# Kernel tuning notes

Measured on AMD Instinct MI355X. Metric: run time of the kernel, lower is better.

The kernel has to match this reference:

```python
import jax, jax.numpy as jnp
import numpy as np

B, DIM, H, W = 16, 512, 32, 32
C = 256          # internal channels = int(512*0.5)
HEADS = 4        # max(1, 256//64)
KD = 32          # key_dim = int(64*0.5)
HD = 64          # head_dim = 256//4
SCALE = KD ** -0.5


def _silu(x):
    return x * jax.nn.sigmoid(x)


def conv1x1(x, Wm, s, b, act):
    # 1x1 conv + folded eval-mode BN (scale/shift) + optional SiLU
    y = jnp.einsum('bchw,oc->bohw', x, Wm)
    y = y * s[None, :, None, None] + b[None, :, None, None]
    return _silu(y) if act else y


def dwconv3(x, Wd, s, b):
    # depthwise 3x3 conv (groups = channels) + BN scale/shift, no act
    y = jax.lax.conv_general_dilated(
        x, Wd, window_strides=(1, 1), padding='SAME',
        feature_group_count=x.shape[1],
        dimension_numbers=('NCHW', 'OIHW', 'NCHW'))
    return y * s[None, :, None, None] + b[None, :, None, None]


def _mk_conv(key, c_out, c_in, k=1):
    k1, k2, k3 = jax.random.split(key, 3)
    fan_in = c_in * k * k
    if k == 1:
        Wm = jax.random.normal(k1, (c_out, c_in), jnp.float32) * fan_in ** -0.5
    else:
        Wm = jax.random.normal(k1, (c_out, c_in, k, k), jnp.float32) * fan_in ** -0.5
    s = jax.random.uniform(k2, (c_out,), jnp.float32, 0.5, 1.5)
    b = 0.1 * jax.random.normal(k3, (c_out,), jnp.float32)
    return Wm, s, b


def setup_inputs() -> dict:
    key = jax.random.key(0)
    ks = jax.random.split(key, 8)
    x = jax.random.normal(ks[0], (B, DIM, H, W), jnp.float32)
    W_cv1, s_cv1, b_cv1 = _mk_conv(ks[1], 2 * C, DIM)
    W_qkv, s_qkv, b_qkv = _mk_conv(ks[2], C + 2 * HEADS * KD, C)  # 512 out
    W_proj, s_proj, b_proj = _mk_conv(ks[3], C, C)
    # depthwise 3x3: OIHW with I=1, groups=C
    W_pe, s_pe, b_pe = _mk_conv(ks[4], C, 1, k=3)
    W_ffn1, s_ffn1, b_ffn1 = _mk_conv(ks[5], 2 * C, C)
    W_ffn2, s_ffn2, b_ffn2 = _mk_conv(ks[6], C, 2 * C)
    W_cv2, s_cv2, b_cv2 = _mk_conv(ks[7], DIM, 2 * C)
    return {
        'x': x,
        'W_cv1': W_cv1, 's_cv1': s_cv1, 'b_cv1': b_cv1,
        'W_qkv': W_qkv, 's_qkv': s_qkv, 'b_qkv': b_qkv,
        'W_proj': W_proj, 's_proj': s_proj, 'b_proj': b_proj,
        'W_pe': W_pe, 's_pe': s_pe, 'b_pe': b_pe,
        'W_ffn1': W_ffn1, 's_ffn1': s_ffn1, 'b_ffn1': b_ffn1,
        'W_ffn2': W_ffn2, 's_ffn2': s_ffn2, 'b_ffn2': b_ffn2,
        'W_cv2': W_cv2, 's_cv2': s_cv2, 'b_cv2': b_cv2,
    }


def reference(x,
              W_cv1, s_cv1, b_cv1,
              W_qkv, s_qkv, b_qkv,
              W_proj, s_proj, b_proj,
              W_pe, s_pe, b_pe,
              W_ffn1, s_ffn1, b_ffn1,
              W_ffn2, s_ffn2, b_ffn2,
              W_cv2, s_cv2, b_cv2):
    bsz, _, h, w = x.shape
    n = h * w
    y = conv1x1(x, W_cv1, s_cv1, b_cv1, act=True)          # [b, 2C, h, w]
    a, bb = y[:, :C], y[:, C:]

    # ----- Attention on bb -----
    qkv = conv1x1(bb, W_qkv, s_qkv, b_qkv, act=False)       # [b, 2*h*kd + C, h, w]
    qkv = qkv.reshape(bsz, HEADS, 2 * KD + HD, n)
    q, k, v = qkv[:, :, :KD], qkv[:, :, KD:2 * KD], qkv[:, :, 2 * KD:]
    attn = jnp.einsum('bhdn,bhdm->bhnm', q, k) * SCALE      # [b, heads, n, n]
    attn = jax.nn.softmax(attn, axis=-1)
    xa = jnp.einsum('bhdm,bhnm->bhdn', v, attn).reshape(bsz, C, h, w)
    xa = xa + dwconv3(v.reshape(bsz, C, h, w), W_pe, s_pe, b_pe)
    xa = conv1x1(xa, W_proj, s_proj, b_proj, act=False)
    bb = bb + xa

    # ----- FFN on bb -----
    ff = conv1x1(bb, W_ffn1, s_ffn1, b_ffn1, act=True)
    ff = conv1x1(ff, W_ffn2, s_ffn2, b_ffn2, act=False)
    bb = bb + ff

    return conv1x1(jnp.concatenate([a, bb], axis=1), W_cv2, s_cv2, b_cv2, act=True)
```

## Files before the change

kernel.cpp:

```cpp
#include <hip/hip_runtime.h>

typedef unsigned short u16;
typedef __attribute__((ext_vector_type(8))) short short8;
typedef __attribute__((ext_vector_type(4))) float f32x4;
typedef __attribute__((ext_vector_type(4))) unsigned int uint4v;
typedef __attribute__((ext_vector_type(4))) unsigned short ushort4v;

#define N_PIX 1024
constexpr float SCALE = 0.17677669529663687f;

__device__ __forceinline__ float bf2f(u16 v) {
    unsigned u = ((unsigned)v) << 16;
    return __builtin_bit_cast(float, u);
}
__device__ __forceinline__ u16 f2bf(float f) {
    unsigned u = __builtin_bit_cast(unsigned, f);
    u += 0x7fff + ((u >> 16) & 1);
    return (u16)(u >> 16);
}
__device__ __forceinline__ float silu_f(float x) { return x / (1.f + __expf(-x)); }

__device__ __forceinline__ f32x4 mfma16(short8 a, short8 b, f32x4 c) {
    return __builtin_amdgcn_mfma_f32_16x16x32_bf16(a, b, c, 0, 0, 0);
}

__device__ __forceinline__ void gl_lds16(const u16* g, u16* l) {
    __builtin_amdgcn_global_load_lds(
        (const __attribute__((address_space(1))) unsigned int*)g,
        (__attribute__((address_space(3))) unsigned int*)l, 16, 0, 0);
}

__global__ void cvtw_k(const float* s0, u16* d0, int n0,
                       const float* s1, u16* d1, int n1,
                       const float* s2, u16* d2, int n2,
                       const float* s3, u16* d3, int n3,
                       const float* s4, u16* d4, int n4,
                       const float* s5, u16* d5, int n5)
{
    const float* sp = nullptr; u16* dp = nullptr; int n = 0;
    switch (blockIdx.y) {
        case 0: sp = s0; dp = d0; n = n0; break;
        case 1: sp = s1; dp = d1; n = n1; break;
        case 2: sp = s2; dp = d2; n = n2; break;
        case 3: sp = s3; dp = d3; n = n3; break;
        case 4: sp = s4; dp = d4; n = n4; break;
        case 5: sp = s5; dp = d5; n = n5; break;
    }
    for (int i = blockIdx.x * 256 + threadIdx.x; i < n; i += gridDim.x * 256)
        dp[i] = f2bf(sp[i]);
}

__global__ __launch_bounds__(256) void trans_k(const float* __restrict__ x, u16* __restrict__ xt)
{
    __shared__ float LT[64 * 65];
    const int tid = threadIdx.x;
    const int n0 = blockIdx.x * 64;
    const int c0 = blockIdx.y * 64;
    const int b  = blockIdx.z;
    const int w = tid >> 6, ln = tid & 63;
#pragma unroll
    for (int s = 0; s < 16; ++s) {
        int c = s * 4 + w;
        LT[c * 65 + ln] = x[((size_t)(b * 512 + c0 + c)) * N_PIX + n0 + ln];
    }
    __syncthreads();
#pragma unroll
    for (int s = 0; s < 16; ++s) {
        int n = s * 4 + w;
        xt[((size_t)(b * N_PIX + n0 + n)) * 512 + c0 + ln] = f2bf(LT[ln * 65 + n]);
    }
}

__global__ __launch_bounds__(256) void gemm_k(
    const u16* __restrict__ Xt, int xcs, int xcoff,
    const u16* __restrict__ Wb, int Cin,
    const float* __restrict__ sc, const float* __restrict__ bi,
    const u16* __restrict__ res, int rcs, int rcoff,
    u16* __restrict__ out, int ocs, int ocoff,
    float* __restrict__ out32,
    u16* __restrict__ vsep,
    int act)
{
    __shared__ __align__(16) u16 WT[2][128 * 32];
    __shared__ __align__(16) u16 XT[2][128 * 32];
    const int tid  = threadIdx.x;
    const int lane = tid & 63;
    const int w    = __builtin_amdgcn_readfirstlane(tid >> 6);
    const int wr = w >> 1, wc = w & 1;
    const int n0 = blockIdx.x * 128;
    const int o0 = blockIdx.y * 128;
    const int b  = blockIdx.z;
    const int l4 = lane >> 4, l15 = lane & 15;

    const int srow0 = w * 16 + (lane >> 2);
    const int srow1 = (w + 4) * 16 + (lane >> 2);
    const int skc   = (lane & 3) * 8;
    const u16* wg0 = Wb + (size_t)(o0 + srow0) * Cin + skc;
    const u16* wg1 = Wb + (size_t)(o0 + srow1) * Cin + skc;
    const u16* xg0 = Xt + ((size_t)(b * N_PIX + n0 + srow0)) * xcs + xcoff + skc;
    const u16* xg1 = Xt + ((size_t)(b * N_PIX + n0 + srow1)) * xcs + xcoff + skc;

    f32x4 acc[4][4];
#pragma unroll
    for (int i = 0; i < 4; ++i)
#pragma unroll
        for (int j = 0; j < 4; ++j) acc[i][j] = (f32x4){0.f, 0.f, 0.f, 0.f};

    const int nk = Cin >> 5;
    gl_lds16(wg0, &WT[0][w * 512]);
    gl_lds16(wg1, &WT[0][(w + 4) * 512]);
    gl_lds16(xg0, &XT[0][w * 512]);
    gl_lds16(xg1, &XT[0][(w + 4) * 512]);
    __syncthreads();

    for (int kk = 0; kk < nk; ++kk) {
        const int cur = kk & 1;
        if (kk + 1 < nk) {
            const int cc = (kk + 1) << 5;
            gl_lds16(wg0 + cc, &WT[cur ^ 1][w * 512]);
            gl_lds16(wg1 + cc, &WT[cur ^ 1][(w + 4) * 512]);
            gl_lds16(xg0 + cc, &XT[cur ^ 1][w * 512]);
            gl_lds16(xg1 + cc, &XT[cur ^ 1][(w + 4) * 512]);
        }
        short8 af[4], bfr[4];
#pragma unroll
        for (int i = 0; i < 4; ++i)
            af[i] = *(const short8*)&WT[cur][(wr * 64 + i * 16 + l15) * 32 + l4 * 8];
#pragma unroll
        for (int j = 0; j < 4; ++j)
            bfr[j] = *(const short8*)&XT[cur][(wc * 64 + j * 16 + l15) * 32 + l4 * 8];
#pragma unroll
        for (int i = 0; i < 4; ++i)
#pragma unroll
            for (int j = 0; j < 4; ++j)
                acc[i][j] = mfma16(af[i], bfr[j], acc[i][j]);
        __syncthreads();
    }

    const bool is_v = (vsep != nullptr) && (wr == 1);
#pragma unroll
    for (int i = 0; i < 4; ++i) {
        const int ob = o0 + wr * 64 + i * 16 + l4 * 4;
        float s4[4], b4[4];
#pragma unroll
        for (int r = 0; r < 4; ++r) { s4[r] = sc[ob + r]; b4[r] = bi[ob + r]; }
#pragma unroll
        for (int j = 0; j < 4; ++j) {
            const int n = n0 + wc * 64 + j * 16 + l15;
            float v[4];
#pragma unroll
            for (int r = 0; r < 4; ++r) {
                v[r] = acc[i][j][r] * s4[r] + b4[r];
                if (act) v[r] = silu_f(v[r]);
            }
            if (out32) {
                const int Cout = gridDim.y * 128;
#pragma unroll
                for (int r = 0; r < 4; ++r)
                    out32[((size_t)b * Cout + ob + r) * N_PIX + n] = v[r];
            } else if (is_v) {
                const int hh = ob >> 7;
                const int dv = (ob & 127) - 64;
                u16* vp = vsep + (((size_t)(b * 4 + hh)) * 64 + dv) * N_PIX + n;
#pragma unroll
                for (int r = 0; r < 4; ++r) vp[r * N_PIX] = f2bf(v[r]);
            } else {
                const size_t base = ((size_t)(b * N_PIX + n)) * ocs + ocoff + ob;
                if (res) {
                    ushort4v rr = *(const ushort4v*)&res[((size_t)(b * N_PIX + n)) * rcs + rcoff + ob];
#pragma unroll
                    for (int r = 0; r < 4; ++r) v[r] += bf2f(rr[r]);
                }
                ushort4v pk;
#pragma unroll
                for (int r = 0; r < 4; ++r) pk[r] = f2bf(v[r]);
                *(ushort4v*)&out[base] = pk;
            }
        }
    }
}

__global__ __launch_bounds__(256) void attn_k(
    const u16* __restrict__ qkvt, const u16* __restrict__ vsep,
    u16* __restrict__ xat)
{
    __shared__ __align__(16) u16 KT[128 * 40];
    __shared__ __align__(16) u16 VT[64 * 136];
    __shared__ __align__(16) u16 PL[4 * 16 * 136];
    const int tid  = threadIdx.x;
    const int lane = tid & 63;
    const int w    = __builtin_amdgcn_readfirstlane(tid >> 6);
    const int l4 = lane >> 4, l15 = lane & 15;
    const int h = blockIdx.y, b = blockIdx.z;
    const int n0w = blockIdx.x * 64 + w * 16;
    u16* PLw = PL + w * 16 * 136;

    const short8 qf = *(const short8*)&qkvt[((size_t)(b * N_PIX + n0w + l15)) * 512 + h * 128 + l4 * 8];

    float mrun[4], lrun[4];
#pragma unroll
    for (int r = 0; r < 4; ++r) { mrun[r] = -1e30f; lrun[r] = 0.f; }
    f32x4 accv[4];
#pragma unroll
    for (int d = 0; d < 4; ++d) accv[d] = (f32x4){0.f, 0.f, 0.f, 0.f};
    const f32x4 z4 = {0.f, 0.f, 0.f, 0.f};

    const int smr = tid >> 2, skc = (tid & 3) * 8;
    const int sdv = tid >> 4, sg = (tid & 15) * 8;

    for (int t8 = 0; t8 < 8; ++t8) {
        const int m0 = t8 * 128;
        *(uint4v*)&KT[smr * 40 + skc] =
            *(const uint4v*)&qkvt[((size_t)(b * N_PIX + m0 + smr)) * 512 + h * 128 + 32 + skc];
        *(uint4v*)&KT[(smr + 64) * 40 + skc] =
            *(const uint4v*)&qkvt[((size_t)(b * N_PIX + m0 + 64 + smr)) * 512 + h * 128 + 32 + skc];
#pragma unroll
        for (int rr = 0; rr < 4; ++rr)
            *(uint4v*)&VT[(rr * 16 + sdv) * 136 + sg] =
                *(const uint4v*)&vsep[(((size_t)(b * 4 + h)) * 64 + rr * 16 + sdv) * N_PIX + m0 + sg];
        __syncthreads();

        f32x4 s[8];
#pragma unroll
        for (int mt = 0; mt < 8; ++mt) {
            short8 kf = *(const short8*)&KT[(mt * 16 + l15) * 40 + l4 * 8];
            s[mt] = mfma16(qf, kf, z4);
        }
        float tm[4];
#pragma unroll
        for (int r = 0; r < 4; ++r) {
            float m_ = s[0][r];
#pragma unroll
            for (int mt = 1; mt < 8; ++mt) m_ = fmaxf(m_, s[mt][r]);
            m_ = fmaxf(m_, __shfl_xor(m_, 1));
            m_ = fmaxf(m_, __shfl_xor(m_, 2));
            m_ = fmaxf(m_, __shfl_xor(m_, 4));
            m_ = fmaxf(m_, __shfl_xor(m_, 8));
            tm[r] = m_ * SCALE;
        }
#pragma unroll
        for (int r = 0; r < 4; ++r) {
            float mnew = fmaxf(mrun[r], tm[r]);
            float corr = __expf(mrun[r] - mnew);
            mrun[r] = mnew;
            lrun[r] *= corr;
#pragma unroll
            for (int d = 0; d < 4; ++d) accv[d][r] *= corr;
        }
#pragma unroll
        for (int mt = 0; mt < 8; ++mt)
#pragma unroll
            for (int r = 0; r < 4; ++r) {
                float p = __expf(s[mt][r] * SCALE - mrun[r]);
                lrun[r] += p;
                PLw[(l4 * 4 + r) * 136 + mt * 16 + l15] = f2bf(p);
            }
#pragma unroll
        for (int mq = 0; mq < 4; ++mq) {
            short8 pa = *(const short8*)&PLw[l15 * 136 + mq * 32 + l4 * 8];
#pragma unroll
            for (int d = 0; d < 4; ++d) {
                short8 vf = *(const short8*)&VT[(d * 16 + l15) * 136 + mq * 32 + l4 * 8];
                accv[d] = mfma16(pa, vf, accv[d]);
            }
        }
        __syncthreads();
    }

#pragma unroll
    for (int r = 0; r < 4; ++r) {
        float sum = lrun[r];
        sum += __shfl_xor(sum, 1);
        sum += __shfl_xor(sum, 2);
        sum += __shfl_xor(sum, 4);
        sum += __shfl_xor(sum, 8);
        lrun[r] = 1.f / sum;
    }
#pragma unroll
    for (int d = 0; d < 4; ++d)
#pragma unroll
        for (int r = 0; r < 4; ++r) {
            const int n = n0w + l4 * 4 + r;
            xat[((size_t)(b * N_PIX + n)) * 256 + h * 64 + d * 16 + l15] =
                f2bf(accv[d][r] * lrun[r]);
        }
}

__global__ __launch_bounds__(256) void pe_k(
    const u16* __restrict__ vsep, const float* __restrict__ Wpe,
    const float* __restrict__ spe, const float* __restrict__ bpe,
    u16* __restrict__ xat)
{
    const int t  = threadIdx.x;
    const int y0 = blockIdx.x * 2;
    const int b  = blockIdx.y;
    const u16* vp = vsep + ((size_t)(b * 256 + t)) * N_PIX;

    float rv[128];
#pragma unroll
    for (int rr = 0; rr < 4; ++rr) {
        const int yy = y0 - 1 + rr;
        if (yy >= 0 && yy < 32) {
#pragma unroll
            for (int g = 0; g < 4; ++g) {
                uint4v u = *(const uint4v*)&vp[yy * 32 + g * 8];
#pragma unroll
                for (int e = 0; e < 4; ++e) {
                    rv[rr * 32 + g * 8 + e * 2]     = bf2f((u16)(u[e] & 0xffff));
                    rv[rr * 32 + g * 8 + e * 2 + 1] = bf2f((u16)(u[e] >> 16));
                }
            }
        } else {
#pragma unroll
            for (int j = 0; j < 32; ++j) rv[rr * 32 + j] = 0.f;
        }
    }
    float w9[9];
#pragma unroll
    for (int i = 0; i < 9; ++i) w9[i] = Wpe[t * 9 + i];
    const float scv = spe[t], biv = bpe[t];
    u16* xp = xat + ((size_t)(b * N_PIX)) * 256 + t;

#pragma unroll
    for (int py = 0; py < 2; ++py)
#pragma unroll
        for (int px = 0; px < 32; ++px) {
            float a = 0.f;
#pragma unroll
            for (int ky = 0; ky < 3; ++ky) {
                const int lr = py + ky;
#pragma unroll
                for (int kx = 0; kx < 3; ++kx) {
                    const int xx = px + kx - 1;
                    if (xx >= 0 && xx < 32)
                        a = fmaf(w9[ky * 3 + kx], rv[lr * 32 + xx], a);
                }
            }
            const int n = (y0 + py) * 32 + px;
            u16* p = xp + (size_t)n * 256;
            *p = f2bf(bf2f(*p) + a * scv + biv);
        }
}

extern "C" void kernel_launch(void* const* d_in, const int* in_sizes, int n_in,
                              void* d_out, int out_size, void* d_ws, size_t ws_size,
                              hipStream_t stream)
{
    const float* x      = (const float*)d_in[0];
    const float* W_cv1  = (const float*)d_in[1];
    const float* s_cv1  = (const float*)d_in[2];
    const float* b_cv1  = (const float*)d_in[3];
    const float* W_qkv  = (const float*)d_in[4];
    const float* s_qkv  = (const float*)d_in[5];
    const float* b_qkv  = (const float*)d_in[6];
    const float* W_proj = (const float*)d_in[7];
    const float* s_proj = (const float*)d_in[8];
    const float* b_proj = (const float*)d_in[9];
    const float* W_pe   = (const float*)d_in[10];
    const float* s_pe   = (const float*)d_in[11];
    const float* b_pe   = (const float*)d_in[12];
    const float* W_ffn1 = (const float*)d_in[13];
    const float* s_ffn1 = (const float*)d_in[14];
    const float* b_ffn1 = (const float*)d_in[15];
    const float* W_ffn2 = (const float*)d_in[16];
    const float* s_ffn2 = (const float*)d_in[17];
    const float* b_ffn2 = (const float*)d_in[18];
    const float* W_cv2  = (const float*)d_in[19];
    const float* s_cv2  = (const float*)d_in[20];
    const float* b_cv2  = (const float*)d_in[21];

    u16* ws = (u16*)d_ws;
    u16* xt      = ws;
    u16* yt      = xt + 8388608;
    u16* qkvt    = yt + 8388608;
    u16* fft     = qkvt + 8388608;
    u16* vsep    = fft + 8388608;
    u16* xat     = vsep + 4194304;
    u16* wb_cv1  = xat + 4194304;
    u16* wb_qkv  = wb_cv1 + 262144;
    u16* wb_proj = wb_qkv + 131072;
    u16* wb_ffn1 = wb_proj + 65536;
    u16* wb_ffn2 = wb_ffn1 + 131072;
    u16* wb_cv2  = wb_ffn2 + 131072;

    cvtw_k<<<dim3(64, 6), 256, 0, stream>>>(
        W_cv1, wb_cv1, 512 * 512, W_qkv, wb_qkv, 512 * 256,
        W_proj, wb_proj, 256 * 256, W_ffn1, wb_ffn1, 512 * 256,
        W_ffn2, wb_ffn2, 256 * 512, W_cv2, wb_cv2, 512 * 512);
    trans_k<<<dim3(16, 8, 16), 256, 0, stream>>>(x, xt);

    gemm_k<<<dim3(8, 4, 16), 256, 0, stream>>>(
        xt, 512, 0, wb_cv1, 512, s_cv1, b_cv1,
        nullptr, 0, 0, yt, 512, 0, nullptr, nullptr, 1);
    gemm_k<<<dim3(8, 4, 16), 256, 0, stream>>>(
        yt, 512, 256, wb_qkv, 256, s_qkv, b_qkv,
        nullptr, 0, 0, qkvt, 512, 0, nullptr, vsep, 0);
    attn_k<<<dim3(16, 4, 16), 256, 0, stream>>>(qkvt, vsep, xat);
    pe_k<<<dim3(16, 16), 256, 0, stream>>>(vsep, W_pe, s_pe, b_pe, xat);
    gemm_k<<<dim3(8, 2, 16), 256, 0, stream>>>(
        xat, 256, 0, wb_proj, 256, s_proj, b_proj,
        yt, 512, 256, yt, 512, 256, nullptr, nullptr, 0);
    gemm_k<<<dim3(8, 4, 16), 256, 0, stream>>>(
        yt, 512, 256, wb_ffn1, 256, s_ffn1, b_ffn1,
        nullptr, 0, 0, fft, 512, 0, nullptr, nullptr, 1);
    gemm_k<<<dim3(8, 2, 16), 256, 0, stream>>>(
        fft, 512, 0, wb_ffn2, 512, s_ffn2, b_ffn2,
        yt, 512, 256, yt, 512, 256, nullptr, nullptr, 0);
    gemm_k<<<dim3(8, 4, 16), 256, 0, stream>>>(
        yt, 512, 0, wb_cv2, 512, s_cv2, b_cv2,
        nullptr, 0, 0, nullptr, 0, 0, (float*)d_out, nullptr, 1);
}
```

Baseline: 303.0 us.

## Double-buffer K/V tiles in attention with register prefetch and one barrier

Restructures the attention loop to process 64-key tiles in 16 steps instead of 128-key tiles in 8. K/V tiles are double-buffered in LDS, and the next tile's global loads are prefetched into registers while the current tile is computed. This drops the second __syncthreads per iteration, aiming to hide global-load latency and cut barrier stalls. It also adds s_setprio around the MFMA sections; the cost is more loop iterations and more online-softmax rescaling steps.

```diff
diff --git a/kernel.cpp b/kernel.cpp
--- a/kernel.cpp
+++ b/kernel.cpp
@@ -184,18 +184,23 @@
     const u16* __restrict__ qkvt, const u16* __restrict__ vsep,
     u16* __restrict__ xat)
 {
-    __shared__ __align__(16) u16 KT[128 * 40];
-    __shared__ __align__(16) u16 VT[64 * 136];
-    __shared__ __align__(16) u16 PL[4 * 16 * 136];
+    __shared__ __align__(16) u16 KT[2][64 * 40];
+    __shared__ __align__(16) u16 VT[2][64 * 72];
+    __shared__ __align__(16) u16 PL[4 * 16 * 72];
     const int tid  = threadIdx.x;
     const int lane = tid & 63;
     const int w    = __builtin_amdgcn_readfirstlane(tid >> 6);
     const int l4 = lane >> 4, l15 = lane & 15;
     const int h = blockIdx.y, b = blockIdx.z;
     const int n0w = blockIdx.x * 64 + w * 16;
-    u16* PLw = PL + w * 16 * 136;
+    u16* PLw = PL + w * 16 * 72;
 
     const short8 qf = *(const short8*)&qkvt[((size_t)(b * N_PIX + n0w + l15)) * 512 + h * 128 + l4 * 8];
+
+    const int skr = tid >> 2, skc = (tid & 3) * 8;
+    const int svd = tid >> 3, svm = (tid & 7) * 8;
+    const u16* kgbase = qkvt + ((size_t)(b * N_PIX + skr)) * 512 + h * 128 + 32 + skc;
+    const u16* vgbase = vsep + (((size_t)(b * 4 + h)) * 64 + svd) * N_PIX + svm;
 
     float mrun[4], lrun[4];
 #pragma unroll
@@ -205,33 +210,36 @@
     for (int d = 0; d < 4; ++d) accv[d] = (f32x4){0.f, 0.f, 0.f, 0.f};
     const f32x4 z4 = {0.f, 0.f, 0.f, 0.f};
 
-    const int smr = tid >> 2, skc = (tid & 3) * 8;
-    const int sdv = tid >> 4, sg = (tid & 15) * 8;
-
-    for (int t8 = 0; t8 < 8; ++t8) {
-        const int m0 = t8 * 128;
-        *(uint4v*)&KT[smr * 40 + skc] =
-            *(const uint4v*)&qkvt[((size_t)(b * N_PIX + m0 + smr)) * 512 + h * 128 + 32 + skc];
-        *(uint4v*)&KT[(smr + 64) * 40 + skc] =
-            *(const uint4v*)&qkvt[((size_t)(b * N_PIX + m0 + 64 + smr)) * 512 + h * 128 + 32 + skc];
-#pragma unroll
-        for (int rr = 0; rr < 4; ++rr)
-            *(uint4v*)&VT[(rr * 16 + sdv) * 136 + sg] =
-                *(const uint4v*)&vsep[(((size_t)(b * 4 + h)) * 64 + rr * 16 + sdv) * N_PIX + m0 + sg];
+    uint4v kreg = *(const uint4v*)(kgbase);
+    uint4v vr0  = *(const uint4v*)(vgbase);
+    uint4v vr1  = *(const uint4v*)(vgbase + 32 * N_PIX);
+
+    for (int t = 0; t < 16; ++t) {
+        const int cur = t & 1;
+        *(uint4v*)&KT[cur][skr * 40 + skc] = kreg;
+        *(uint4v*)&VT[cur][svd * 72 + svm] = vr0;
+        *(uint4v*)&VT[cur][(svd + 32) * 72 + svm] = vr1;
+        if (t < 15) {
+            const int m1 = (t + 1) * 64;
+            kreg = *(const uint4v*)(kgbase + (size_t)m1 * 512);
+            vr0  = *(const uint4v*)(vgbase + m1);
+            vr1  = *(const uint4v*)(vgbase + 32 * N_PIX + m1);
+        }
         __syncthreads();
 
-        f32x4 s[8];
-#pragma unroll
-        for (int mt = 0; mt < 8; ++mt) {
-            short8 kf = *(const short8*)&KT[(mt * 16 + l15) * 40 + l4 * 8];
+        f32x4 s[4];
+        __builtin_amdgcn_s_setprio(1);
+#pragma unroll
+        for (int mt = 0; mt < 4; ++mt) {
+            short8 kf = *(const short8*)&KT[cur][(mt * 16 + l15) * 40 + l4 * 8];
             s[mt] = mfma16(qf, kf, z4);
         }
+        __builtin_amdgcn_s_setprio(0);
+
         float tm[4];
 #pragma unroll
         for (int r = 0; r < 4; ++r) {
-            float m_ = s[0][r];
-#pragma unroll
-            for (int mt = 1; mt < 8; ++mt) m_ = fmaxf(m_, s[mt][r]);
+            float m_ = fmaxf(fmaxf(s[0][r], s[1][r]), fmaxf(s[2][r], s[3][r]));
             m_ = fmaxf(m_, __shfl_xor(m_, 1));
             m_ = fmaxf(m_, __shfl_xor(m_, 2));
             m_ = fmaxf(m_, __shfl_xor(m_, 4));
@@ -248,23 +256,25 @@
             for (int d = 0; d < 4; ++d) accv[d][r] *= corr;
         }
 #pragma unroll
-        for (int mt = 0; mt < 8; ++mt)
+        for (int mt = 0; mt < 4; ++mt)
 #pragma unroll
             for (int r = 0; r < 4; ++r) {
                 float p = __expf(s[mt][r] * SCALE - mrun[r]);
                 lrun[r] += p;
-                PLw[(l4 * 4 + r) * 136 + mt * 16 + l15] = f2bf(p);
-            }
-#pragma unroll
-        for (int mq = 0; mq < 4; ++mq) {
-            short8 pa = *(const short8*)&PLw[l15 * 136 + mq * 32 + l4 * 8];
+                PLw[(l4 * 4 + r) * 72 + mt * 16 + l15] = f2bf(p);
+            }
+
+        __builtin_amdgcn_s_setprio(1);
+#pragma unroll
+        for (int mq = 0; mq < 2; ++mq) {
+            short8 pa = *(const short8*)&PLw[l15 * 72 + mq * 32 + l4 * 8];
 #pragma unroll
             for (int d = 0; d < 4; ++d) {
-                short8 vf = *(const short8*)&VT[(d * 16 + l15) * 136 + mq * 32 + l4 * 8];
+                short8 vf = *(const short8*)&VT[cur][(d * 16 + l15) * 72 + mq * 32 + l4 * 8];
                 accv[d] = mfma16(pa, vf, accv[d]);
             }
         }
-        __syncthreads();
+        __builtin_amdgcn_s_setprio(0);
     }
 
 #pragma unroll
```

Measured after the change: 284.2 us. -6.2%, faster.
